# Kernel tuning notes

Hardware: AMD Instinct MI355X
Metric: run time of the kernel (lower is better)

Reference implementation:

```python
import jax, jax.numpy as jnp
import numpy as np


def _k_hot(tokens, vocab_size, pad_id):
    """Count-vector (sum of one-hots, pad rows zeroed) over the last axis.

    tokens: int array [..., L] -> float32 [..., vocab_size]
    Equivalent to torch: onehot(tokens, N=V, ignore_index=pad).sum(-2).float(),
    but via scatter-add (no [., L, V] materialization).
    """
    lead = tokens.shape[:-1]
    flat = tokens.reshape(-1, tokens.shape[-1])
    w = (flat != pad_id).astype(jnp.float32)

    def one_row(t, m):
        return jnp.zeros((vocab_size,), jnp.float32).at[t].add(m)

    counts = jax.vmap(one_row)(flat, w)
    return counts.reshape(lead + (vocab_size,))


def setup_inputs() -> dict:
    key = jax.random.key(0)
    k1, k2 = jax.random.split(key)
    B, C, Lc, Ls, V = 64, 16, 64, 48, 32000
    candidates = jax.random.randint(k1, (B, C, Lc), 0, V, dtype=jnp.int64)
    src_tokens = jax.random.randint(k2, (B, Ls), 0, V, dtype=jnp.int64)
    return {"candidates": candidates, "src_tokens": src_tokens,
            "vocab_size": V, "pad_id": 0}


def reference(candidates, src_tokens, vocab_size, pad_id):
    # k-hot count vectors
    refs_k_hot = _k_hot(src_tokens, vocab_size, pad_id)[:, None, :]   # [B, 1, V]
    cand_k_hot = _k_hot(candidates, vocab_size, pad_id)               # [B, C, V]

    # cosine similarity -> distance score = 1 - cos
    dots = jnp.einsum('bov,bcv->bc', refs_k_hot, cand_k_hot)          # [B, C]
    denom = jnp.linalg.norm(refs_k_hot, axis=-1) * jnp.linalg.norm(cand_k_hot, axis=-1)
    scores = 1.0 - dots / denom                                       # [B, C]

    # sort descending (as in the torch code) and gather candidates
    order = jnp.argsort(-scores, axis=-1)                             # [B, C]
    sorted_scores = jnp.take_along_axis(scores, order, axis=-1)
    sorted_cands = jnp.take_along_axis(candidates, order[:, :, None], axis=1)

    output = sorted_cands[:, 0, :]                                    # top1=True
    out_lengths = jnp.sum(output != pad_id, axis=-1)
    return (output, out_lengths, sorted_scores)
```

## Files before the change

### kernel.cpp

```cpp
#include <hip/hip_runtime.h>
#include <math.h>

#define NB 64
#define NC 16
#define LC 64
#define LS 48

__global__ void ngram_scores_kernel(const int* __restrict__ cand,
                                    const int* __restrict__ src,
                                    const int* __restrict__ pad_ptr,
                                    float* __restrict__ scores) {
    const int bc   = blockIdx.x;
    const int b    = bc / NC;
    const int lane = threadIdx.x;
    const int pad  = pad_ptr[0];

    __shared__ int s_src[LS];
    __shared__ int s_cand[LC];
    if (lane < LS) s_src[lane] = src[b * LS + lane];
    s_cand[lane] = cand[bc * LC + lane];
    __syncthreads();

    int rn = 0;
    if (lane < LS) {
        const int t = s_src[lane];
        if (t != pad) {
            #pragma unroll
            for (int j = 0; j < LS; ++j) rn += (s_src[j] == t);
        }
    }

    int cn = 0, dt = 0;
    {
        const int t = s_cand[lane];
        if (t != pad) {
            #pragma unroll
            for (int j = 0; j < LC; ++j) cn += (s_cand[j] == t);
            #pragma unroll
            for (int j = 0; j < LS; ++j) dt += (s_src[j] == t);
        }
    }

    #pragma unroll
    for (int off = 32; off > 0; off >>= 1) {
        rn += __shfl_down(rn, off, 64);
        cn += __shfl_down(cn, off, 64);
        dt += __shfl_down(dt, off, 64);
    }

    if (lane == 0) {
        const float denom = sqrtf((float)rn) * sqrtf((float)cn);
        scores[bc] = 1.0f - (float)dt / denom;
    }
}

__global__ void ngram_finalize_kernel(const int* __restrict__ cand,
                                      const int* __restrict__ pad_ptr,
                                      const float* __restrict__ scores,
                                      float* __restrict__ out) {
    const int b    = blockIdx.x;
    const int lane = threadIdx.x;
    const int pad  = pad_ptr[0];

    __shared__ float s_sc[NC];
    __shared__ int   s_best;
    if (lane < NC) s_sc[lane] = scores[b * NC + lane];
    __syncthreads();

    if (lane < NC) {
        const float s = s_sc[lane];
        int rank = 0;
        #pragma unroll
        for (int j = 0; j < NC; ++j) {
            const float t = s_sc[j];
            rank += (t > s) || (t == s && j < lane);
        }
        out[NB * LC + NB + b * NC + rank] = s;
        if (rank == 0) s_best = lane;
    }
    __syncthreads();

    const int best = s_best;
    const int tok  = cand[(b * NC + best) * LC + lane];
    out[b * LC + lane] = (float)tok;

    const unsigned long long m = __ballot(tok != pad);
    if (lane == 0) out[NB * LC + b] = (float)__popcll(m);
}

extern "C" void kernel_launch(void* const* d_in, const int* in_sizes, int n_in,
                              void* d_out, int out_size, void* d_ws, size_t ws_size,
                              hipStream_t stream) {
    const int* cand = (const int*)d_in[0];
    const int* src  = (const int*)d_in[1];
    const int* pad  = (const int*)d_in[3];

    float* scores = (float*)d_ws;
    float* out    = (float*)d_out;

    ngram_scores_kernel<<<NB * NC, 64, 0, stream>>>(cand, src, pad, scores);
    ngram_finalize_kernel<<<NB, 64, 0, stream>>>(cand, pad, scores, out);
}
```

Measured before the change: 11.67 us.

## Fuse score and finalize kernels into one block per batch row

```diff
diff --git a/kernel.cpp b/kernel.cpp
--- a/kernel.cpp
+++ b/kernel.cpp
@@ -6,19 +6,24 @@
 #define LC 64
 #define LS 48
 
-__global__ void ngram_scores_kernel(const int* __restrict__ cand,
-                                    const int* __restrict__ src,
-                                    const int* __restrict__ pad_ptr,
-                                    float* __restrict__ scores) {
-    const int bc   = blockIdx.x;
-    const int b    = bc / NC;
-    const int lane = threadIdx.x;
+__global__ __launch_bounds__(NC * 64) void ngram_fused_kernel(
+        const int* __restrict__ cand,
+        const int* __restrict__ src,
+        const int* __restrict__ pad_ptr,
+        float* __restrict__ out) {
+    const int b    = blockIdx.x;
+    const int tid  = threadIdx.x;
+    const int wave = tid >> 6;
+    const int lane = tid & 63;
     const int pad  = pad_ptr[0];
 
-    __shared__ int s_src[LS];
-    __shared__ int s_cand[LC];
-    if (lane < LS) s_src[lane] = src[b * LS + lane];
-    s_cand[lane] = cand[bc * LC + lane];
+    __shared__ int   s_src[LS];
+    __shared__ int   s_cand[NC][LC];
+    __shared__ float s_sc[NC];
+    __shared__ int   s_best;
+
+    if (tid < LS) s_src[tid] = src[b * LS + tid];
+    s_cand[wave][lane] = cand[(b * NC + wave) * LC + lane];
     __syncthreads();
 
     int rn = 0;
@@ -32,10 +37,10 @@
 
     int cn = 0, dt = 0;
     {
-        const int t = s_cand[lane];
+        const int t = s_cand[wave][lane];
         if (t != pad) {
             #pragma unroll
-            for (int j = 0; j < LC; ++j) cn += (s_cand[j] == t);
+            for (int j = 0; j < LC; ++j) cn += (s_cand[wave][j] == t);
             #pragma unroll
             for (int j = 0; j < LS; ++j) dt += (s_src[j] == t);
         }
@@ -50,42 +55,29 @@
 
     if (lane == 0) {
         const float denom = sqrtf((float)rn) * sqrtf((float)cn);
-        scores[bc] = 1.0f - (float)dt / denom;
+        s_sc[wave] = 1.0f - (float)dt / denom;
     }
-}
-
-__global__ void ngram_finalize_kernel(const int* __restrict__ cand,
-                                      const int* __restrict__ pad_ptr,
-                                      const float* __restrict__ scores,
-                                      float* __restrict__ out) {
-    const int b    = blockIdx.x;
-    const int lane = threadIdx.x;
-    const int pad  = pad_ptr[0];
-
-    __shared__ float s_sc[NC];
-    __shared__ int   s_best;
-    if (lane < NC) s_sc[lane] = scores[b * NC + lane];
     __syncthreads();
 
-    if (lane < NC) {
-        const float s = s_sc[lane];
+    if (tid < NC) {
+        const float s = s_sc[tid];
         int rank = 0;
         #pragma unroll
         for (int j = 0; j < NC; ++j) {
             const float t = s_sc[j];
-            rank += (t > s) || (t == s && j < lane);
+            rank += (t > s) || (t == s && j < tid);
         }
         out[NB * LC + NB + b * NC + rank] = s;
-        if (rank == 0) s_best = lane;
+        if (rank == 0) s_best = tid;
     }
     __syncthreads();
 
-    const int best = s_best;
-    const int tok  = cand[(b * NC + best) * LC + lane];
-    out[b * LC + lane] = (float)tok;
-
-    const unsigned long long m = __ballot(tok != pad);
-    if (lane == 0) out[NB * LC + b] = (float)__popcll(m);
+    if (wave == 0) {
+        const int tok = s_cand[s_best][lane];
+        out[b * LC + lane] = (float)tok;
+        const unsigned long long m = __ballot(tok != pad);
+        if (lane == 0) out[NB * LC + b] = (float)__popcll(m);
+    }
 }
 
 extern "C" void kernel_launch(void* const* d_in, const int* in_sizes, int n_in,
@@ -95,9 +87,7 @@
     const int* src  = (const int*)d_in[1];
     const int* pad  = (const int*)d_in[3];
 
-    float* scores = (float*)d_ws;
-    float* out    = (float*)d_out;
+    float* out = (float*)d_out;
 
-    ngram_scores_kernel<<<NB * NC, 64, 0, stream>>>(cand, src, pad, scores);
-    ngram_finalize_kernel<<<NB, 64, 0, stream>>>(cand, pad, scores, out);
+    ngram_fused_kernel<<<NB, NC * 64, 0, stream>>>(cand, src, pad, out);
 }
```

Measured after the change: 10.51 us. -10.0%, faster.
